# Kernel tuning notes

Hardware: AMD Instinct MI355X
Metric: run time of the kernel (lower is better)

Reference implementation:

```python
import jax, jax.numpy as jnp
import numpy as np

NUM_USERS = 1_000_000
NUM_ITEMS = 1_000_000
EMBED_DIM = 32
BATCH = 131072
LAYER_SIZES = [96, 64]  # MLP: 96->64 (ReLU) -> 64->1 (ReLU)


def setup_inputs() -> dict:
    key = jax.random.key(0)
    ks = jax.random.split(key, 8)
    scale = 1.0 / EMBED_DIM  # ScaledEmbedding init std
    user_ids = jax.random.randint(ks[0], (BATCH,), 0, NUM_USERS)
    item_ids = jax.random.randint(ks[1], (BATCH,), 0, NUM_ITEMS)
    U_w = jax.random.normal(ks[2], (NUM_USERS, EMBED_DIM), jnp.float32) * scale
    Q_w = jax.random.normal(ks[3], (NUM_ITEMS, EMBED_DIM), jnp.float32) * scale
    # ZeroEmbedding biases init to zero; use tiny random so grads/outputs are non-trivial
    A_w = jnp.zeros((NUM_USERS, 1), jnp.float32)
    B_w = jnp.zeros((NUM_ITEMS, 1), jnp.float32)
    # nn.Linear default init ~ U(-1/sqrt(fan_in), 1/sqrt(fan_in))
    lim1 = 1.0 / np.sqrt(LAYER_SIZES[0])
    lim2 = 1.0 / np.sqrt(LAYER_SIZES[1])
    W1 = jax.random.uniform(ks[4], (LAYER_SIZES[1], LAYER_SIZES[0]), jnp.float32, -lim1, lim1)
    b1 = jax.random.uniform(ks[5], (LAYER_SIZES[1],), jnp.float32, -lim1, lim1)
    W2 = jax.random.uniform(ks[6], (1, LAYER_SIZES[1]), jnp.float32, -lim2, lim2)
    b2 = jax.random.uniform(ks[7], (1,), jnp.float32, -lim2, lim2)
    return {"user_ids": user_ids, "item_ids": item_ids, "U_w": U_w, "Q_w": Q_w,
            "A_w": A_w, "B_w": B_w, "W1": W1, "b1": b1, "W2": W2, "b2": b2}


def reference(user_ids, item_ids, U_w, Q_w, A_w, B_w, W1, b1, W2, b2):
    u = U_w[user_ids]            # [B, D] gather
    q = Q_w[item_ids]            # [B, D]
    a = A_w[user_ids]            # [B, 1]
    b = B_w[item_ids]            # [B, 1]
    uq = u * q                   # [B, D]
    # diag(u @ q.T) == row-wise dot product sum(u*q, axis=1)
    predictions = jnp.sum(uq, axis=1, keepdims=True) + a + b  # [B, 1]
    x = jnp.concatenate([u, q, uq], axis=1)                   # [B, 3D]
    h = jax.nn.relu(x @ W1.T + b1)                            # [B, 64]
    score = jax.nn.relu(h @ W2.T + b2)                        # [B, 1]
    return predictions.squeeze(-1), score.squeeze(-1)
```

## Files before the change

### kernel.cpp

```cpp
#include <hip/hip_runtime.h>

#define BLK 256
#define DIM 32

typedef __attribute__((ext_vector_type(8))) short bf16x8;
typedef __attribute__((ext_vector_type(4))) float f32x4;

__device__ __forceinline__ unsigned short f2bf(float f) {
    unsigned u = __float_as_uint(f);
    unsigned r = ((u >> 16) & 1u) + 0x7fffu;
    return (unsigned short)((u + r) >> 16);
}

__global__ __launch_bounds__(BLK, 6) void mtn_fused(
    const int* __restrict__ uid, const int* __restrict__ iid,
    const float* __restrict__ Uw, const float* __restrict__ Qw,
    const float* __restrict__ Aw, const float* __restrict__ Bw,
    const float* __restrict__ W1, const float* __restrict__ b1g,
    const float* __restrict__ W2, const float* __restrict__ b2g,
    float* __restrict__ out, int batch)
{
    __shared__ __align__(16) unsigned short Bp[3 * 4 * 64 * 8];

    const int t    = threadIdx.x;
    const int lane = t & 63;
    const int wave = t >> 6;
    const int lr   = lane & 15;
    const int h    = lane >> 4;

    const int s = blockIdx.x * 64 + wave * 16 + lr;
    const bool valid = (s < batch);
    const int u_idx = valid ? uid[s] : 0;
    const int q_idx = valid ? iid[s] : 0;

    const float4* up = (const float4*)(Uw + (long long)u_idx * DIM + h * 8);
    const float4* qp = (const float4*)(Qw + (long long)q_idx * DIM + h * 8);
    float4 uv0 = up[0], uv1 = up[1];
    float4 qv0 = qp[0], qv1 = qp[1];
    float av = 0.f;
    if (h == 0) av = Aw[u_idx] + Bw[q_idx];

    {
        const float4* w4 = (const float4*)W1;
#pragma unroll
        for (int it = 0; it < 6; ++it) {
            int base4 = t + it * BLK;
            float4 w = w4[base4];
            int lin = base4 * 4;
            float we[4] = {w.x, w.y, w.z, w.w};
#pragma unroll
            for (int e4 = 0; e4 < 4; ++e4) {
                int lidx = lin + e4;
                int j = lidx / 96;
                int k = lidx - j * 96;
                int n  = j >> 4, jr = j & 15;
                int ks = k >> 5, kg = (k >> 3) & 3, e = k & 7;
                int l  = kg * 16 + jr;
                Bp[(((ks * 4 + n) << 6) + l) * 8 + e] = f2bf(we[e4]);
            }
        }
    }

    bf16x8 a0, a1, a2;
    float dotp = 0.f;
    {
        const float ue[8] = {uv0.x,uv0.y,uv0.z,uv0.w, uv1.x,uv1.y,uv1.z,uv1.w};
        const float qe[8] = {qv0.x,qv0.y,qv0.z,qv0.w, qv1.x,qv1.y,qv1.z,qv1.w};
#pragma unroll
        for (int e = 0; e < 8; ++e) {
            float pp = ue[e] * qe[e];
            dotp += pp;
            a0[e] = (short)f2bf(ue[e]);
            a1[e] = (short)f2bf(qe[e]);
            a2[e] = (short)f2bf(pp);
        }
    }
    dotp += __shfl_xor(dotp, 16);
    dotp += __shfl_xor(dotp, 32);
    if (valid && h == 0) out[s] = dotp + av;

    __syncthreads();

    float w2l[4], b1l[4];
#pragma unroll
    for (int n = 0; n < 4; ++n) {
        w2l[n] = W2[n * 16 + lr];
        b1l[n] = b1g[n * 16 + lr];
    }
    const float b2v = b2g[0];

    f32x4 c0 = {b1l[0], b1l[0], b1l[0], b1l[0]};
    f32x4 c1 = {b1l[1], b1l[1], b1l[1], b1l[1]};
    f32x4 c2 = {b1l[2], b1l[2], b1l[2], b1l[2]};
    f32x4 c3 = {b1l[3], b1l[3], b1l[3], b1l[3]};

    const bf16x8* bp = (const bf16x8*)Bp;
    {
        bf16x8 b0 = bp[0 * 64 + lane], b1 = bp[1 * 64 + lane];
        bf16x8 b2 = bp[2 * 64 + lane], b3 = bp[3 * 64 + lane];
        c0 = __builtin_amdgcn_mfma_f32_16x16x32_bf16(a0, b0, c0, 0, 0, 0);
        c1 = __builtin_amdgcn_mfma_f32_16x16x32_bf16(a0, b1, c1, 0, 0, 0);
        c2 = __builtin_amdgcn_mfma_f32_16x16x32_bf16(a0, b2, c2, 0, 0, 0);
        c3 = __builtin_amdgcn_mfma_f32_16x16x32_bf16(a0, b3, c3, 0, 0, 0);
    }
    {
        bf16x8 b0 = bp[4 * 64 + lane], b1 = bp[5 * 64 + lane];
        bf16x8 b2 = bp[6 * 64 + lane], b3 = bp[7 * 64 + lane];
        c0 = __builtin_amdgcn_mfma_f32_16x16x32_bf16(a1, b0, c0, 0, 0, 0);
        c1 = __builtin_amdgcn_mfma_f32_16x16x32_bf16(a1, b1, c1, 0, 0, 0);
        c2 = __builtin_amdgcn_mfma_f32_16x16x32_bf16(a1, b2, c2, 0, 0, 0);
        c3 = __builtin_amdgcn_mfma_f32_16x16x32_bf16(a1, b3, c3, 0, 0, 0);
    }
    {
        bf16x8 b0 = bp[8 * 64 + lane], b1 = bp[9 * 64 + lane];
        bf16x8 b2 = bp[10 * 64 + lane], b3 = bp[11 * 64 + lane];
        c0 = __builtin_amdgcn_mfma_f32_16x16x32_bf16(a2, b0, c0, 0, 0, 0);
        c1 = __builtin_amdgcn_mfma_f32_16x16x32_bf16(a2, b1, c1, 0, 0, 0);
        c2 = __builtin_amdgcn_mfma_f32_16x16x32_bf16(a2, b2, c2, 0, 0, 0);
        c3 = __builtin_amdgcn_mfma_f32_16x16x32_bf16(a2, b3, c3, 0, 0, 0);
    }

    float tot[4];
#pragma unroll
    for (int r = 0; r < 4; ++r) {
        float p = fmaxf(c0[r], 0.f) * w2l[0] + fmaxf(c1[r], 0.f) * w2l[1]
                + fmaxf(c2[r], 0.f) * w2l[2] + fmaxf(c3[r], 0.f) * w2l[3];
        p += __shfl_xor(p, 1);
        p += __shfl_xor(p, 2);
        p += __shfl_xor(p, 4);
        p += __shfl_xor(p, 8);
        tot[r] = p;
    }
    if (lr < 4) {
        int so = blockIdx.x * 64 + wave * 16 + h * 4 + lr;
        if (so < batch) out[batch + so] = fmaxf(tot[lr] + b2v, 0.f);
    }
}

extern "C" void kernel_launch(void* const* d_in, const int* in_sizes, int n_in,
                              void* d_out, int out_size, void* d_ws, size_t ws_size,
                              hipStream_t stream) {
    const int*   uid = (const int*)  d_in[0];
    const int*   iid = (const int*)  d_in[1];
    const float* Uw  = (const float*)d_in[2];
    const float* Qw  = (const float*)d_in[3];
    const float* Aw  = (const float*)d_in[4];
    const float* Bw  = (const float*)d_in[5];
    const float* W1  = (const float*)d_in[6];
    const float* b1  = (const float*)d_in[7];
    const float* W2  = (const float*)d_in[8];
    const float* b2  = (const float*)d_in[9];
    float* out = (float*)d_out;
    int batch = in_sizes[0];

    int blocks = (batch + 63) / 64;
    hipLaunchKernelGGL(mtn_fused, dim3(blocks), dim3(BLK), 0, stream,
                       uid, iid, Uw, Qw, Aw, Bw, W1, b1, W2, b2, out, batch);
}
```

Measured before the change: 19.45 us.

## Process two 16-row tiles per wave to amortize W1 staging

Each wave now handles 32 samples instead of 16, so each block covers 128 rows and the grid is halved. The per-block cost of converting W1 to bf16 and staging it in LDS is spread over twice as many samples, and each B fragment read from LDS feeds two MFMAs. The price is more registers per thread (launch bounds lowered from 6 to 4 blocks per CU) and fewer blocks to hide the latency of the random gathers.

```diff
diff --git a/kernel.cpp b/kernel.cpp
--- a/kernel.cpp
+++ b/kernel.cpp
@@ -12,7 +12,7 @@
     return (unsigned short)((u + r) >> 16);
 }
 
-__global__ __launch_bounds__(BLK, 6) void mtn_fused(
+__global__ __launch_bounds__(BLK, 4) void mtn_fused(
     const int* __restrict__ uid, const int* __restrict__ iid,
     const float* __restrict__ Uw, const float* __restrict__ Qw,
     const float* __restrict__ Aw, const float* __restrict__ Bw,
@@ -28,17 +28,26 @@
     const int lr   = lane & 15;
     const int h    = lane >> 4;
 
-    const int s = blockIdx.x * 64 + wave * 16 + lr;
-    const bool valid = (s < batch);
-    const int u_idx = valid ? uid[s] : 0;
-    const int q_idx = valid ? iid[s] : 0;
+    const int base = blockIdx.x * 128 + wave * 32;
+    const int s0 = base + lr;
+    const int s1 = base + 16 + lr;
+    const bool v0 = (s0 < batch), v1 = (s1 < batch);
+    const int u0 = v0 ? uid[s0] : 0, q0i = v0 ? iid[s0] : 0;
+    const int u1 = v1 ? uid[s1] : 0, q1i = v1 ? iid[s1] : 0;
 
-    const float4* up = (const float4*)(Uw + (long long)u_idx * DIM + h * 8);
-    const float4* qp = (const float4*)(Qw + (long long)q_idx * DIM + h * 8);
-    float4 uv0 = up[0], uv1 = up[1];
-    float4 qv0 = qp[0], qv1 = qp[1];
-    float av = 0.f;
-    if (h == 0) av = Aw[u_idx] + Bw[q_idx];
+    const float4* up0 = (const float4*)(Uw + (long long)u0  * DIM + h * 8);
+    const float4* qp0 = (const float4*)(Qw + (long long)q0i * DIM + h * 8);
+    const float4* up1 = (const float4*)(Uw + (long long)u1  * DIM + h * 8);
+    const float4* qp1 = (const float4*)(Qw + (long long)q1i * DIM + h * 8);
+    float4 ua0 = up0[0], ua1 = up0[1];
+    float4 qa0 = qp0[0], qa1 = qp0[1];
+    float4 ub0 = up1[0], ub1 = up1[1];
+    float4 qb0 = qp1[0], qb1 = qp1[1];
+    float av0 = 0.f, av1 = 0.f;
+    if (h == 0) {
+        av0 = Aw[u0] + Bw[q0i];
+        av1 = Aw[u1] + Bw[q1i];
+    }
 
     {
         const float4* w4 = (const float4*)W1;
@@ -61,23 +70,30 @@
         }
     }
 
-    bf16x8 a0, a1, a2;
-    float dotp = 0.f;
+    bf16x8 x0a, x0b, x0c, x1a, x1b, x1c;
+    float d0 = 0.f, d1 = 0.f;
     {
-        const float ue[8] = {uv0.x,uv0.y,uv0.z,uv0.w, uv1.x,uv1.y,uv1.z,uv1.w};
-        const float qe[8] = {qv0.x,qv0.y,qv0.z,qv0.w, qv1.x,qv1.y,qv1.z,qv1.w};
+        const float ue0[8] = {ua0.x,ua0.y,ua0.z,ua0.w, ua1.x,ua1.y,ua1.z,ua1.w};
+        const float qe0[8] = {qa0.x,qa0.y,qa0.z,qa0.w, qa1.x,qa1.y,qa1.z,qa1.w};
+        const float ue1[8] = {ub0.x,ub0.y,ub0.z,ub0.w, ub1.x,ub1.y,ub1.z,ub1.w};
+        const float qe1[8] = {qb0.x,qb0.y,qb0.z,qb0.w, qb1.x,qb1.y,qb1.z,qb1.w};
 #pragma unroll
         for (int e = 0; e < 8; ++e) {
-            float pp = ue[e] * qe[e];
-            dotp += pp;
-            a0[e] = (short)f2bf(ue[e]);
-            a1[e] = (short)f2bf(qe[e]);
-            a2[e] = (short)f2bf(pp);
+            float p0 = ue0[e] * qe0[e];
+            float p1 = ue1[e] * qe1[e];
+            d0 += p0;  d1 += p1;
+            x0a[e] = (short)f2bf(ue0[e]);
+            x0b[e] = (short)f2bf(qe0[e]);
+            x0c[e] = (short)f2bf(p0);
+            x1a[e] = (short)f2bf(ue1[e]);
+            x1b[e] = (short)f2bf(qe1[e]);
+            x1c[e] = (short)f2bf(p1);
         }
     }
-    dotp += __shfl_xor(dotp, 16);
-    dotp += __shfl_xor(dotp, 32);
-    if (valid && h == 0) out[s] = dotp + av;
+    d0 += __shfl_xor(d0, 16);  d0 += __shfl_xor(d0, 32);
+    d1 += __shfl_xor(d1, 16);  d1 += __shfl_xor(d1, 32);
+    if (v0 && h == 0) out[s0] = d0 + av0;
+    if (v1 && h == 0) out[s1] = d1 + av1;
 
     __syncthreads();
 
@@ -89,51 +105,64 @@
     }
     const float b2v = b2g[0];
 
-    f32x4 c0 = {b1l[0], b1l[0], b1l[0], b1l[0]};
-    f32x4 c1 = {b1l[1], b1l[1], b1l[1], b1l[1]};
-    f32x4 c2 = {b1l[2], b1l[2], b1l[2], b1l[2]};
-    f32x4 c3 = {b1l[3], b1l[3], b1l[3], b1l[3]};
+    f32x4 c00 = {b1l[0],b1l[0],b1l[0],b1l[0]}, c01 = {b1l[1],b1l[1],b1l[1],b1l[1]};
+    f32x4 c02 = {b1l[2],b1l[2],b1l[2],b1l[2]}, c03 = {b1l[3],b1l[3],b1l[3],b1l[3]};
+    f32x4 c10 = c00, c11 = c01, c12 = c02, c13 = c03;
 
     const bf16x8* bp = (const bf16x8*)Bp;
     {
-        bf16x8 b0 = bp[0 * 64 + lane], b1 = bp[1 * 64 + lane];
-        bf16x8 b2 = bp[2 * 64 + lane], b3 = bp[3 * 64 + lane];
-        c0 = __builtin_amdgcn_mfma_f32_16x16x32_bf16(a0, b0, c0, 0, 0, 0);
-        c1 = __builtin_amdgcn_mfma_f32_16x16x32_bf16(a0, b1, c1, 0, 0, 0);
-        c2 = __builtin_amdgcn_mfma_f32_16x16x32_bf16(a0, b2, c2, 0, 0, 0);
-        c3 = __builtin_amdgcn_mfma_f32_16x16x32_bf16(a0, b3, c3, 0, 0, 0);
+        bf16x8 b0 = bp[0*64+lane], b1 = bp[1*64+lane], b2 = bp[2*64+lane], b3 = bp[3*64+lane];
+        c00 = __builtin_amdgcn_mfma_f32_16x16x32_bf16(x0a, b0, c00, 0, 0, 0);
+        c10 = __builtin_amdgcn_mfma_f32_16x16x32_bf16(x1a, b0, c10, 0, 0, 0);
+        c01 = __builtin_amdgcn_mfma_f32_16x16x32_bf16(x0a, b1, c01, 0, 0, 0);
+        c11 = __builtin_amdgcn_mfma_f32_16x16x32_bf16(x1a, b1, c11, 0, 0, 0);
+        c02 = __builtin_amdgcn_mfma_f32_16x16x32_bf16(x0a, b2, c02, 0, 0, 0);
+        c12 = __builtin_amdgcn_mfma_f32_16x16x32_bf16(x1a, b2, c12, 0, 0, 0);
+        c03 = __builtin_amdgcn_mfma_f32_16x16x32_bf16(x0a, b3, c03, 0, 0, 0);
+        c13 = __builtin_amdgcn_mfma_f32_16x16x32_bf16(x1a, b3, c13, 0, 0, 0);
     }
     {
-        bf16x8 b0 = bp[4 * 64 + lane], b1 = bp[5 * 64 + lane];
-        bf16x8 b2 = bp[6 * 64 + lane], b3 = bp[7 * 64 + lane];
-        c0 = __builtin_amdgcn_mfma_f32_16x16x32_bf16(a1, b0, c0, 0, 0, 0);
-        c1 = __builtin_amdgcn_mfma_f32_16x16x32_bf16(a1, b1, c1, 0, 0, 0);
-        c2 = __builtin_amdgcn_mfma_f32_16x16x32_bf16(a1, b2, c2, 0, 0, 0);
-        c3 = __builtin_amdgcn_mfma_f32_16x16x32_bf16(a1, b3, c3, 0, 0, 0);
+        bf16x8 b0 = bp[4*64+lane], b1 = bp[5*64+lane], b2 = bp[6*64+lane], b3 = bp[7*64+lane];
+        c00 = __builtin_amdgcn_mfma_f32_16x16x32_bf16(x0b, b0, c00, 0, 0, 0);
+        c10 = __builtin_amdgcn_mfma_f32_16x16x32_bf16(x1b, b0, c10, 0, 0, 0);
+        c01 = __builtin_amdgcn_mfma_f32_16x16x32_bf16(x0b, b1, c01, 0, 0, 0);
+        c11 = __builtin_amdgcn_mfma_f32_16x16x32_bf16(x1b, b1, c11, 0, 0, 0);
+        c02 = __builtin_amdgcn_mfma_f32_16x16x32_bf16(x0b, b2, c02, 0, 0, 0);
+        c12 = __builtin_amdgcn_mfma_f32_16x16x32_bf16(x1b, b2, c12, 0, 0, 0);
+        c03 = __builtin_amdgcn_mfma_f32_16x16x32_bf16(x0b, b3, c03, 0, 0, 0);
+        c13 = __builtin_amdgcn_mfma_f32_16x16x32_bf16(x1b, b3, c13, 0, 0, 0);
     }
     {
-        bf16x8 b0 = bp[8 * 64 + lane], b1 = bp[9 * 64 + lane];
-        bf16x8 b2 = bp[10 * 64 + lane], b3 = bp[11 * 64 + lane];
-        c0 = __builtin_amdgcn_mfma_f32_16x16x32_bf16(a2, b0, c0, 0, 0, 0);
-        c1 = __builtin_amdgcn_mfma_f32_16x16x32_bf16(a2, b1, c1, 0, 0, 0);
-        c2 = __builtin_amdgcn_mfma_f32_16x16x32_bf16(a2, b2, c2, 0, 0, 0);
-        c3 = __builtin_amdgcn_mfma_f32_16x16x32_bf16(a2, b3, c3, 0, 0, 0);
+        bf16x8 b0 = bp[8*64+lane], b1 = bp[9*64+lane], b2 = bp[10*64+lane], b3 = bp[11*64+lane];
+        c00 = __builtin_amdgcn_mfma_f32_16x16x32_bf16(x0c, b0, c00, 0, 0, 0);
+        c10 = __builtin_amdgcn_mfma_f32_16x16x32_bf16(x1c, b0, c10, 0, 0, 0);
+        c01 = __builtin_amdgcn_mfma_f32_16x16x32_bf16(x0c, b1, c01, 0, 0, 0);
+        c11 = __builtin_amdgcn_mfma_f32_16x16x32_bf16(x1c, b1, c11, 0, 0, 0);
+        c02 = __builtin_amdgcn_mfma_f32_16x16x32_bf16(x0c, b2, c02, 0, 0, 0);
+        c12 = __builtin_amdgcn_mfma_f32_16x16x32_bf16(x1c, b2, c12, 0, 0, 0);
+        c03 = __builtin_amdgcn_mfma_f32_16x16x32_bf16(x0c, b3, c03, 0, 0, 0);
+        c13 = __builtin_amdgcn_mfma_f32_16x16x32_bf16(x1c, b3, c13, 0, 0, 0);
     }
 
-    float tot[4];
 #pragma unroll
-    for (int r = 0; r < 4; ++r) {
-        float p = fmaxf(c0[r], 0.f) * w2l[0] + fmaxf(c1[r], 0.f) * w2l[1]
-                + fmaxf(c2[r], 0.f) * w2l[2] + fmaxf(c3[r], 0.f) * w2l[3];
-        p += __shfl_xor(p, 1);
-        p += __shfl_xor(p, 2);
-        p += __shfl_xor(p, 4);
-        p += __shfl_xor(p, 8);
-        tot[r] = p;
-    }
-    if (lr < 4) {
-        int so = blockIdx.x * 64 + wave * 16 + h * 4 + lr;
-        if (so < batch) out[batch + so] = fmaxf(tot[lr] + b2v, 0.f);
+    for (int tile = 0; tile < 2; ++tile) {
+        f32x4 e0 = tile ? c10 : c00, e1 = tile ? c11 : c01;
+        f32x4 e2 = tile ? c12 : c02, e3 = tile ? c13 : c03;
+        float tot[4];
+#pragma unroll
+        for (int r = 0; r < 4; ++r) {
+            float p = fmaxf(e0[r], 0.f) * w2l[0] + fmaxf(e1[r], 0.f) * w2l[1]
+                    + fmaxf(e2[r], 0.f) * w2l[2] + fmaxf(e3[r], 0.f) * w2l[3];
+            p += __shfl_xor(p, 1);
+            p += __shfl_xor(p, 2);
+            p += __shfl_xor(p, 4);
+            p += __shfl_xor(p, 8);
+            tot[r] = p;
+        }
+        if (lr < 4) {
+            int so = base + tile * 16 + h * 4 + lr;
+            if (so < batch) out[batch + so] = fmaxf(tot[lr] + b2v, 0.f);
+        }
     }
 }
 
@@ -153,7 +182,7 @@
     float* out = (float*)d_out;
     int batch = in_sizes[0];
 
-    int blocks = (batch + 63) / 64;
+    int blocks = (batch + 127) / 128;
     hipLaunchKernelGGL(mtn_fused, dim3(blocks), dim3(BLK), 0, stream,
                        uid, iid, Uw, Qw, Aw, Bw, W1, b1, W2, b2, out, batch);
 }
```

Result: faster. 18.61 us (-4.3%).
